# Kernel optimization log

Hardware: AMD Instinct MI355X
Metric: run time of the kernel (lower is better)

The kernel has to match this reference:

```python
import jax, jax.numpy as jnp
import numpy as np

D = 768          # 16*16*3
N = 196
H = 8
HD = D // H      # 96
SCALE = HD ** -0.5
EPS = 1e-5


def _ln(x, s, b):
    m = jnp.mean(x, axis=-1, keepdims=True)
    v = jnp.mean((x - m) ** 2, axis=-1, keepdims=True)
    return (x - m) * jax.lax.rsqrt(v + EPS) * s + b


def setup_inputs() -> dict:
    key = jax.random.key(0)
    ks = jax.random.split(key, 16)
    B = 64
    w = lambda k, shp: (jax.random.normal(k, shp, jnp.float32) * 0.02)
    return {
        "x": jax.random.normal(ks[0], (B, N, D), jnp.float32),
        "x_Eem": jax.random.normal(ks[1], (B, 3, 222, 222), jnp.float32),
        "pos_emb": jax.random.normal(ks[2], (1, N, D), jnp.float32),
        "dw_w": w(ks[3], (3, 1, 16, 16)),     # depthwise conv, groups=3 (OIHW, I=1)
        "dw_b": jnp.zeros((3,), jnp.float32),
        "pw_w": w(ks[4], (D, 3)),             # pointwise 1x1 conv as matrix
        "pw_b": jnp.zeros((D,), jnp.float32),
        "qkv_w": w(ks[5], (3 * D, D)),        # no bias (qkv_bias=False)
        "proj_w": w(ks[6], (D, D)),
        "proj_b": jnp.zeros((D,), jnp.float32),
        "ln1_s": jnp.ones((D,), jnp.float32),
        "ln1_b": jnp.zeros((D,), jnp.float32),
        "ln2_s": jnp.ones((D,), jnp.float32),
        "ln2_b": jnp.zeros((D,), jnp.float32),
        "fc1_w": w(ks[7], (4 * D, D)),
        "fc1_b": jnp.zeros((4 * D,), jnp.float32),
        "fc2_w": w(ks[8], (D, 4 * D)),
        "fc2_b": jnp.zeros((D,), jnp.float32),
    }


def _patch_embed(img, dw_w, dw_b, pw_w, pw_b):
    # depthwise conv: kernel 16, stride 16, padding 1, groups=3
    h = jax.lax.conv_general_dilated(
        img, dw_w, window_strides=(16, 16), padding=[(1, 1), (1, 1)],
        dimension_numbers=("NCHW", "OIHW", "NCHW"), feature_group_count=3)
    h = h + dw_b[None, :, None, None]           # [B,3,14,14]
    h = jnp.einsum("bchw,oc->bohw", h, pw_w) + pw_b[None, :, None, None]
    B = h.shape[0]
    return h.reshape(B, D, N).transpose(0, 2, 1)  # [B,N,D]


def _ve_attention(x, x_emb, qkv_w, proj_w, proj_b):
    B = x.shape[0]
    # pooling gates (AdaptiveMax/AvgPool2d on 3D input pools last two dims)
    maxg = jnp.max(x, axis=(1, 2), keepdims=True)       # [B,1,1]
    maxn = jnp.max(x, axis=2, keepdims=True)            # [B,N,1]
    aveg = jnp.mean(x, axis=(1, 2), keepdims=True)      # [B,1,1]
    aven = jnp.mean(x, axis=2, keepdims=True)           # [B,N,1]
    # F.softmax(maxg*maxn, dim=1); F.softmax(aveg*aven) -> default dim=0 for 3D input
    gate = jax.nn.softmax(maxg * maxn, axis=1) * jax.nn.softmax(aveg * aven, axis=0)
    qkv = jnp.einsum("bnd,ed->bne", x, qkv_w)            # [B,N,3D]
    q = qkv[:, :, :D]
    k = qkv[:, :, D:2 * D]
    v = qkv[:, :, 2 * D:] * gate + x_emb
    to_h = lambda t: t.reshape(B, N, H, HD).transpose(0, 2, 1, 3)  # [B,H,N,hd]
    q, k, v = to_h(q), to_h(k), to_h(v)
    # scores = (q@k^T + v@k^T) * scale == ((q+v)@k^T) * scale
    attn = jax.nn.softmax(jnp.einsum("bhnd,bhmd->bhnm", q + v, k) * SCALE, axis=-1)
    out = jnp.einsum("bhnm,bhmd->bhnd", attn, v)
    out = out.transpose(0, 2, 1, 3).reshape(B, N, D)
    return jnp.einsum("bnd,ed->bne", out, proj_w) + proj_b


def reference(x, x_Eem, pos_emb, dw_w, dw_b, pw_w, pw_b, qkv_w, proj_w, proj_b,
              ln1_s, ln1_b, ln2_s, ln2_b, fc1_w, fc1_b, fc2_w, fc2_b):
    x_emb = _patch_embed(x_Eem, dw_w, dw_b, pw_w, pw_b)
    x = x + pos_emb
    x = x + _ve_attention(_ln(x, ln1_s, ln1_b), x_emb, qkv_w, proj_w, proj_b)
    h = _ln(x, ln2_s, ln2_b)
    h = jax.nn.gelu(jnp.einsum("bnd,fd->bnf", h, fc1_w) + fc1_b, approximate=False)
    h = jnp.einsum("bnf,df->bnd", h, fc2_w) + fc2_b
    return x + h
```

## Files before the change

### kernel.cpp

```cpp
#include <hip/hip_runtime.h>

#define DEV __device__ __forceinline__

typedef __attribute__((ext_vector_type(8))) short short8_t;
typedef __attribute__((ext_vector_type(4))) float float4_t;
typedef __attribute__((ext_vector_type(4))) unsigned short ushort4_t;
typedef __attribute__((ext_vector_type(8))) unsigned short ushort8_t;

#define ATT_SCALE 0.10206207261596577f

DEV unsigned short f2bf(float f) {
  unsigned u = __float_as_uint(f);
  u += 0x7fffu + ((u >> 16) & 1u);
  return (unsigned short)(u >> 16);
}
DEV float bf2f(unsigned short h) { return __uint_as_float(((unsigned)h) << 16); }

DEV float4_t mfma16(short8_t a, short8_t b, float4_t c) {
  return __builtin_amdgcn_mfma_f32_16x16x32_bf16(a, b, c, 0, 0, 0);
}

DEV void gl_lds16(const void* g, void* l) {
  __builtin_amdgcn_global_load_lds((__attribute__((address_space(1))) void*)g,
                                   (__attribute__((address_space(3))) void*)l, 16, 0, 0);
}

__global__ __launch_bounds__(256) void cvt_kernel(const float* __restrict__ w0,
    const float* __restrict__ w1, const float* __restrict__ w2, const float* __restrict__ w3,
    unsigned short* __restrict__ d0, unsigned short* __restrict__ d1,
    unsigned short* __restrict__ d2, unsigned short* __restrict__ d3) {
  const int i = blockIdx.x * 256 + threadIdx.x;
  const float* s;
  unsigned short* d;
  int j;
  if (i < 442368) { s = w0; d = d0; j = i; }
  else if (i < 589824) { s = w1; d = d1; j = i - 442368; }
  else if (i < 1179648) { s = w2; d = d2; j = i - 589824; }
  else { s = w3; d = d3; j = i - 1179648; }
  float4_t v = ((const float4_t*)s)[j];
  ushort4_t o = {f2bf(v[0]), f2bf(v[1]), f2bf(v[2]), f2bf(v[3])};
  ((ushort4_t*)d)[j] = o;
}

__global__ __launch_bounds__(256) void dwconv_kernel(const float* __restrict__ img,
    const float* __restrict__ wgt, const float* __restrict__ wb, float* __restrict__ h3) {
  __shared__ float wsm[256];
  const int bc = blockIdx.x;
  const int c = bc % 3;
  const int tid = threadIdx.x;
  wsm[tid] = wgt[c * 256 + tid];
  __syncthreads();
  if (tid < 196) {
    const int ph = tid / 14, pwv = tid % 14;
    const float* ip = img + (size_t)bc * (222 * 222);
    float acc = 0.f;
#pragma unroll
    for (int i = 0; i < 16; ++i) {
      const int r = ph * 16 - 1 + i;
      if ((unsigned)r < 222u) {
        const float* rp = ip + r * 222;
#pragma unroll
        for (int j = 0; j < 16; ++j) {
          const int cc = pwv * 16 - 1 + j;
          if ((unsigned)cc < 222u) acc += rp[cc] * wsm[i * 16 + j];
        }
      }
    }
    h3[(size_t)bc * 196 + tid] = acc + wb[c];
  }
}

__global__ __launch_bounds__(256) void ln1_kernel(const float* __restrict__ x,
    const float* __restrict__ pos, const float* __restrict__ sG, const float* __restrict__ bG,
    unsigned short* __restrict__ xln, float* __restrict__ maxn, float* __restrict__ aven) {
  __shared__ float rA[4], rB[4], rC[4], rD[4];
  const int row = blockIdx.x, tid = threadIdx.x;
  const int n = row % 196;
  const float* xr = x + (size_t)row * 768;
  const float* pr = pos + (size_t)n * 768;
  float v0 = xr[tid] + pr[tid];
  float v1 = xr[tid + 256] + pr[tid + 256];
  float v2 = xr[tid + 512] + pr[tid + 512];
  float sm = v0 + v1 + v2;
  float sq = v0 * v0 + v1 * v1 + v2 * v2;
  for (int o = 32; o; o >>= 1) { sm += __shfl_xor(sm, o); sq += __shfl_xor(sq, o); }
  if ((tid & 63) == 0) { rA[tid >> 6] = sm; rB[tid >> 6] = sq; }
  __syncthreads();
  const float mean = (rA[0] + rA[1] + rA[2] + rA[3]) * (1.f / 768.f);
  const float var = (rB[0] + rB[1] + rB[2] + rB[3]) * (1.f / 768.f) - mean * mean;
  const float rstd = rsqrtf(var + 1e-5f);
  float y0 = (v0 - mean) * rstd * sG[tid] + bG[tid];
  float y1 = (v1 - mean) * rstd * sG[tid + 256] + bG[tid + 256];
  float y2 = (v2 - mean) * rstd * sG[tid + 512] + bG[tid + 512];
  unsigned short* xo = xln + (size_t)row * 768;
  xo[tid] = f2bf(y0); xo[tid + 256] = f2bf(y1); xo[tid + 512] = f2bf(y2);
  float mx = fmaxf(y0, fmaxf(y1, y2));
  float sy = y0 + y1 + y2;
  for (int o = 32; o; o >>= 1) { mx = fmaxf(mx, __shfl_xor(mx, o)); sy += __shfl_xor(sy, o); }
  if ((tid & 63) == 0) { rC[tid >> 6] = mx; rD[tid >> 6] = sy; }
  __syncthreads();
  if (tid == 0) {
    maxn[row] = fmaxf(fmaxf(rC[0], rC[1]), fmaxf(rC[2], rC[3]));
    aven[row] = (rD[0] + rD[1] + rD[2] + rD[3]) * (1.f / 768.f);
  }
}

__global__ __launch_bounds__(256) void ln2_kernel(const float* __restrict__ x2,
    const float* __restrict__ sG, const float* __restrict__ bG, unsigned short* __restrict__ h2) {
  __shared__ float rA[4], rB[4];
  const int row = blockIdx.x, tid = threadIdx.x;
  const float* xr = x2 + (size_t)row * 768;
  float v0 = xr[tid], v1 = xr[tid + 256], v2 = xr[tid + 512];
  float sm = v0 + v1 + v2;
  float sq = v0 * v0 + v1 * v1 + v2 * v2;
  for (int o = 32; o; o >>= 1) { sm += __shfl_xor(sm, o); sq += __shfl_xor(sq, o); }
  if ((tid & 63) == 0) { rA[tid >> 6] = sm; rB[tid >> 6] = sq; }
  __syncthreads();
  const float mean = (rA[0] + rA[1] + rA[2] + rA[3]) * (1.f / 768.f);
  const float var = (rB[0] + rB[1] + rB[2] + rB[3]) * (1.f / 768.f) - mean * mean;
  const float rstd = rsqrtf(var + 1e-5f);
  unsigned short* xo = h2 + (size_t)row * 768;
  xo[tid]       = f2bf((v0 - mean) * rstd * sG[tid] + bG[tid]);
  xo[tid + 256] = f2bf((v1 - mean) * rstd * sG[tid + 256] + bG[tid + 256]);
  xo[tid + 512] = f2bf((v2 - mean) * rstd * sG[tid + 512] + bG[tid + 512]);
}

__global__ __launch_bounds__(256) void gate1_kernel(const float* __restrict__ maxn,
    const float* __restrict__ aven, float* __restrict__ aveg, float* __restrict__ s1) {
  __shared__ float rA[4], rB[4], rC[4], rD[4];
  const int b = blockIdx.x, tid = threadIdx.x;
  const bool ok = tid < 196;
  const float mv = ok ? maxn[b * 196 + tid] : -1e30f;
  const float av = ok ? aven[b * 196 + tid] : 0.f;
  float m = mv, sa = av;
  for (int o = 32; o; o >>= 1) { m = fmaxf(m, __shfl_xor(m, o)); sa += __shfl_xor(sa, o); }
  if ((tid & 63) == 0) { rA[tid >> 6] = m; rB[tid >> 6] = sa; }
  __syncthreads();
  const float maxg = fmaxf(fmaxf(rA[0], rA[1]), fmaxf(rA[2], rA[3]));
  const float avg = (rB[0] + rB[1] + rB[2] + rB[3]) * (1.f / 196.f);
  if (tid == 0) aveg[b] = avg;
  const float t1 = ok ? maxg * mv : -1e30f;
  float m2 = t1;
  for (int o = 32; o; o >>= 1) m2 = fmaxf(m2, __shfl_xor(m2, o));
  if ((tid & 63) == 0) rC[tid >> 6] = m2;
  __syncthreads();
  const float m2g = fmaxf(fmaxf(rC[0], rC[1]), fmaxf(rC[2], rC[3]));
  const float e = ok ? __expf(t1 - m2g) : 0.f;
  float se = e;
  for (int o = 32; o; o >>= 1) se += __shfl_xor(se, o);
  if ((tid & 63) == 0) rD[tid >> 6] = se;
  __syncthreads();
  const float seg = rD[0] + rD[1] + rD[2] + rD[3];
  if (ok) s1[b * 196 + tid] = e / seg;
}

__global__ __launch_bounds__(64) void gate2_kernel(const float* __restrict__ aveg,
    const float* __restrict__ aven, const float* __restrict__ s1, float* __restrict__ gate) {
  const int n = blockIdx.x, bb = threadIdx.x;
  const float t2 = aveg[bb] * aven[bb * 196 + n];
  float m = t2;
  for (int o = 32; o; o >>= 1) m = fmaxf(m, __shfl_xor(m, o));
  const float e = __expf(t2 - m);
  float ssum = e;
  for (int o = 32; o; o >>= 1) ssum += __shfl_xor(ssum, o);
  gate[bb * 196 + n] = s1[bb * 196 + n] * e / ssum;
}

enum { M_QKV = 0, M_PROJ = 1, M_GELU = 2, M_FC2 = 3 };

template <int MODE>
__global__ __launch_bounds__(256, 2) void gemm_bt(
    const unsigned short* __restrict__ A, const unsigned short* __restrict__ W,
    int K, int Nd,
    const float* __restrict__ bias,
    const float* __restrict__ res0, const float* __restrict__ res1,
    const float* __restrict__ gate, const float* __restrict__ h3,
    const float* __restrict__ pw, const float* __restrict__ pwb,
    unsigned short* __restrict__ oQ, unsigned short* __restrict__ oK,
    unsigned short* __restrict__ oV,
    float* __restrict__ oF, unsigned short* __restrict__ oB) {
  __shared__ __align__(16) unsigned short smem[8192];
  const int tid = threadIdx.x;
  const int w = tid >> 6, lane = tid & 63;
  const int l15 = lane & 15, quad = lane >> 4;
  const int n0 = blockIdx.x * 128, m0 = blockIdx.y * 128;

  const int row0 = tid >> 2;
  const int kc = (((tid & 3) ^ ((tid >> 3) & 3)) << 3);
  const size_t arow0 = (size_t)(m0 + row0) * K + kc;
  const size_t arow1 = (size_t)(m0 + 64 + row0) * K + kc;
  const size_t brow0 = (size_t)(n0 + row0) * K + kc;
  const size_t brow1 = (size_t)(n0 + 64 + row0) * K + kc;
  char* sb = (char*)smem;
  const int ldsA0 = w * 1024, ldsA1 = 4096 + w * 1024;
  const int ldsB0 = 8192 + w * 1024, ldsB1 = 12288 + w * 1024;

  float4_t acc[4][4];
#pragma unroll
  for (int i = 0; i < 4; ++i)
#pragma unroll
    for (int j = 0; j < 4; ++j) acc[i][j] = (float4_t){0.f, 0.f, 0.f, 0.f};

  const int wm = (w >> 1) << 6, wn = (w & 1) << 6;
  const unsigned short* as_ = smem;
  const unsigned short* bs_ = smem + 4096;
  const int squad = quad ^ ((l15 >> 1) & 3);

  for (int kt = 0; kt < K; kt += 32) {
    gl_lds16(A + arow0 + kt, sb + ldsA0);
    gl_lds16(A + arow1 + kt, sb + ldsA1);
    gl_lds16(W + brow0 + kt, sb + ldsB0);
    gl_lds16(W + brow1 + kt, sb + ldsB1);
    __syncthreads();
    short8_t af[4], bfr[4];
#pragma unroll
    for (int mi = 0; mi < 4; ++mi)
      af[mi] = *(const short8_t*)(as_ + (wm + mi * 16 + l15) * 32 + squad * 8);
#pragma unroll
    for (int ni = 0; ni < 4; ++ni)
      bfr[ni] = *(const short8_t*)(bs_ + (wn + ni * 16 + l15) * 32 + squad * 8);
#pragma unroll
    for (int mi = 0; mi < 4; ++mi)
#pragma unroll
      for (int ni = 0; ni < 4; ++ni)
        acc[mi][ni] = mfma16(bfr[ni], af[mi], acc[mi][ni]);
    __syncthreads();
  }

  if (MODE == M_QKV) {
    const int sel = n0 / 768;
    unsigned short* dst = (sel == 0) ? oQ : (sel == 1) ? oK : oV;
    const int nb = n0 - sel * 768 + wn;
#pragma unroll
    for (int mi = 0; mi < 4; ++mi) {
      const int m = m0 + wm + mi * 16 + l15;
      float gv = 0.f, h30 = 0.f, h31 = 0.f, h32 = 0.f;
      if (sel == 2) {
        const int b = m / 196, n = m - b * 196;
        gv = gate[m];
        h30 = h3[(b * 3 + 0) * 196 + n];
        h31 = h3[(b * 3 + 1) * 196 + n];
        h32 = h3[(b * 3 + 2) * 196 + n];
      }
      unsigned short* orow = dst + (size_t)m * 768;
#pragma unroll
      for (int ni = 0; ni < 4; ++ni) {
        const int dcol = nb + ni * 16 + quad * 4;
        ushort4_t st;
        if (sel == 2) {
          const float4_t pwf0 = *(const float4_t*)(pw + dcol * 3);
          const float4_t pwf1 = *(const float4_t*)(pw + dcol * 3 + 4);
          const float4_t pwf2 = *(const float4_t*)(pw + dcol * 3 + 8);
          const float4_t pbf = *(const float4_t*)(pwb + dcol);
          float pwflat[12] = {pwf0[0], pwf0[1], pwf0[2], pwf0[3], pwf1[0], pwf1[1],
                              pwf1[2], pwf1[3], pwf2[0], pwf2[1], pwf2[2], pwf2[3]};
#pragma unroll
          for (int r = 0; r < 4; ++r) {
            const float v = acc[mi][ni][r] * gv + h30 * pwflat[3 * r] +
                            h31 * pwflat[3 * r + 1] + h32 * pwflat[3 * r + 2] + pbf[r];
            st[r] = f2bf(v);
          }
        } else {
#pragma unroll
          for (int r = 0; r < 4; ++r) st[r] = f2bf(acc[mi][ni][r]);
        }
        *(ushort4_t*)(orow + dcol) = st;
      }
    }
  } else if (MODE == M_PROJ || MODE == M_FC2) {
#pragma unroll
    for (int mi = 0; mi < 4; ++mi) {
      const int m = m0 + wm + mi * 16 + l15;
      const int nseq = m % 196;
      const float* rr0 = res0 + (size_t)m * 768;
      const float* rr1 = (MODE == M_PROJ) ? res1 + (size_t)nseq * 768 : nullptr;
      float* oo = oF + (size_t)m * 768;
#pragma unroll
      for (int ni = 0; ni < 4; ++ni) {
        const int col = n0 + wn + ni * 16 + quad * 4;
        const float4_t bb = *(const float4_t*)(bias + col);
        const float4_t r0v = *(const float4_t*)(rr0 + col);
        float4_t v;
#pragma unroll
        for (int r = 0; r < 4; ++r) v[r] = acc[mi][ni][r] + bb[r] + r0v[r];
        if (MODE == M_PROJ) {
          const float4_t r1v = *(const float4_t*)(rr1 + col);
#pragma unroll
          for (int r = 0; r < 4; ++r) v[r] += r1v[r];
        }
        *(float4_t*)(oo + col) = v;
      }
    }
  } else {
#pragma unroll
    for (int mi = 0; mi < 4; ++mi) {
      const int m = m0 + wm + mi * 16 + l15;
      unsigned short* oo = oB + (size_t)m * Nd;
#pragma unroll
      for (int ni = 0; ni < 4; ++ni) {
        const int col = n0 + wn + ni * 16 + quad * 4;
        const float4_t bb = *(const float4_t*)(bias + col);
        ushort4_t st;
#pragma unroll
        for (int r = 0; r < 4; ++r) {
          const float t = acc[mi][ni][r] + bb[r];
          st[r] = f2bf(0.5f * t * (1.f + erff(t * 0.70710678118654752f)));
        }
        *(ushort4_t*)(oo + col) = st;
      }
    }
  }
}

__global__ __launch_bounds__(256) void vtrans_kernel(const unsigned short* __restrict__ vg,
                                                     unsigned short* __restrict__ vt) {
  __shared__ unsigned short lds[96 * 226];
  const int bh = blockIdx.x, b = bh >> 3, h = bh & 7;
  const int tid = threadIdx.x;
  const unsigned short* base = vg + (size_t)(b * 196) * 768 + h * 96;
  for (int idx = tid; idx < 196 * 12; idx += 256) {
    const int n = idx / 12, c = idx % 12;
    const ushort8_t rv = *(const ushort8_t*)(base + (size_t)n * 768 + c * 8);
#pragma unroll
    for (int j = 0; j < 8; ++j) lds[(c * 8 + j) * 226 + n] = rv[j];
  }
  __syncthreads();
  unsigned short* ob = vt + (size_t)bh * (96 * 224);
  for (int idx = tid; idx < 96 * 28; idx += 256) {
    const int d = idx / 28, c = idx % 28;
    const int nn = c * 8;
    ushort8_t o;
#pragma unroll
    for (int j = 0; j < 8; ++j) o[j] = (nn + j < 196) ? lds[d * 226 + nn + j] : (unsigned short)0;
    *(ushort8_t*)(ob + (size_t)d * 224 + nn) = o;
  }
}

__global__ __launch_bounds__(256, 2) void attn_kernel(
    const unsigned short* __restrict__ qg, const unsigned short* __restrict__ vg,
    const unsigned short* __restrict__ kg, const unsigned short* __restrict__ vt,
    unsigned short* __restrict__ att) {
  __shared__ __align__(16) unsigned short p_s[4][16][232];
  const int bh = blockIdx.x, b = bh >> 3, h = bh & 7;
  const int tid = threadIdx.x, w = tid >> 6, lane = tid & 63;
  const int l15 = lane & 15, quad = lane >> 4;
  const unsigned short* qb = qg + (size_t)(b * 196) * 768 + h * 96;
  const unsigned short* vb = vg + (size_t)(b * 196) * 768 + h * 96;
  const unsigned short* kb = kg + (size_t)(b * 196) * 768 + h * 96;
  const unsigned short* vtb = vt + (size_t)bh * (96 * 224);
  for (int i = lane; i < 256; i += 64) p_s[w][i >> 4][208 + (i & 15)] = 0;

  for (int qt = w; qt < 13; qt += 4) {
    const size_t qoff = (size_t)(qt * 16 + l15) * 768 + quad * 8;
    short8_t a0, a1, a2;
    {
      const ushort8_t q0 = *(const ushort8_t*)(qb + qoff);
      const ushort8_t q1 = *(const ushort8_t*)(qb + qoff + 32);
      const ushort8_t q2 = *(const ushort8_t*)(qb + qoff + 64);
      const ushort8_t v0 = *(const ushort8_t*)(vb + qoff);
      const ushort8_t v1 = *(const ushort8_t*)(vb + qoff + 32);
      const ushort8_t v2 = *(const ushort8_t*)(vb + qoff + 64);
#pragma unroll
      for (int j = 0; j < 8; ++j) {
        a0[j] = (short)f2bf(bf2f(q0[j]) + bf2f(v0[j]));
        a1[j] = (short)f2bf(bf2f(q1[j]) + bf2f(v1[j]));
        a2[j] = (short)f2bf(bf2f(q2[j]) + bf2f(v2[j]));
      }
    }
    float4_t S[13];
#pragma unroll
    for (int c = 0; c < 13; ++c) S[c] = (float4_t){0.f, 0.f, 0.f, 0.f};
#pragma unroll
    for (int c = 0; c < 13; ++c) {
      const unsigned short* kr = kb + (size_t)(c * 16 + l15) * 768 + quad * 8;
      S[c] = mfma16(a0, *(const short8_t*)(kr), S[c]);
      S[c] = mfma16(a1, *(const short8_t*)(kr + 32), S[c]);
      S[c] = mfma16(a2, *(const short8_t*)(kr + 64), S[c]);
    }
    float mx[4] = {-1e30f, -1e30f, -1e30f, -1e30f};
#pragma unroll
    for (int c = 0; c < 13; ++c) {
      const bool okc = (c * 16 + l15) < 196;
#pragma unroll
      for (int r = 0; r < 4; ++r) {
        const float v = S[c][r] * ATT_SCALE;
        S[c][r] = okc ? v : -1e30f;
        mx[r] = fmaxf(mx[r], S[c][r]);
      }
    }
#pragma unroll
    for (int o = 1; o <= 8; o <<= 1)
#pragma unroll
      for (int r = 0; r < 4; ++r) mx[r] = fmaxf(mx[r], __shfl_xor(mx[r], o));
    float sum[4] = {0.f, 0.f, 0.f, 0.f};
#pragma unroll
    for (int c = 0; c < 13; ++c)
#pragma unroll
      for (int r = 0; r < 4; ++r) {
        const float e = __expf(S[c][r] - mx[r]);
        S[c][r] = e;
        sum[r] += e;
      }
#pragma unroll
    for (int o = 1; o <= 8; o <<= 1)
#pragma unroll
      for (int r = 0; r < 4; ++r) sum[r] += __shfl_xor(sum[r], o);
    float inv[4];
#pragma unroll
    for (int r = 0; r < 4; ++r) inv[r] = 1.f / sum[r];
#pragma unroll
    for (int c = 0; c < 13; ++c)
#pragma unroll
      for (int r = 0; r < 4; ++r)
        p_s[w][quad * 4 + r][c * 16 + l15] = f2bf(S[c][r] * inv[r]);

    float4_t O[6];
#pragma unroll
    for (int ni = 0; ni < 6; ++ni) O[ni] = (float4_t){0.f, 0.f, 0.f, 0.f};
#pragma unroll
    for (int s = 0; s < 7; ++s) {
      short8_t pa = *(const short8_t*)(&p_s[w][l15][s * 32 + quad * 8]);
#pragma unroll
      for (int ni = 0; ni < 6; ++ni) {
        short8_t vf = *(const short8_t*)(vtb + (size_t)(ni * 16 + l15) * 224 + s * 32 + quad * 8);
        O[ni] = mfma16(vf, pa, O[ni]);
      }
    }
    const int m = qt * 16 + l15;
    if (m < 196) {
      unsigned short* ar = att + (size_t)(b * 196 + m) * 768 + h * 96 + quad * 4;
#pragma unroll
      for (int ni = 0; ni < 6; ++ni) {
        ushort4_t st = {f2bf(O[ni][0]), f2bf(O[ni][1]), f2bf(O[ni][2]), f2bf(O[ni][3])};
        *(ushort4_t*)(ar + ni * 16) = st;
      }
    }
  }
}

extern "C" void kernel_launch(void* const* d_in, const int* in_sizes, int n_in,
                              void* d_out, int out_size, void* d_ws, size_t ws_size,
                              hipStream_t stream) {
  (void)in_sizes; (void)n_in; (void)out_size; (void)ws_size;
  const float* x      = (const float*)d_in[0];
  const float* xE     = (const float*)d_in[1];
  const float* pos    = (const float*)d_in[2];
  const float* dw_w   = (const float*)d_in[3];
  const float* dw_b   = (const float*)d_in[4];
  const float* pw_w   = (const float*)d_in[5];
  const float* pw_b   = (const float*)d_in[6];
  const float* qkv_w  = (const float*)d_in[7];
  const float* proj_w = (const float*)d_in[8];
  const float* proj_b = (const float*)d_in[9];
  const float* ln1_s  = (const float*)d_in[10];
  const float* ln1_b  = (const float*)d_in[11];
  const float* ln2_s  = (const float*)d_in[12];
  const float* ln2_b  = (const float*)d_in[13];
  const float* fc1_w  = (const float*)d_in[14];
  const float* fc1_b  = (const float*)d_in[15];
  const float* fc2_w  = (const float*)d_in[16];
  const float* fc2_b  = (const float*)d_in[17];
  float* out = (float*)d_out;

  char* ws = (char*)d_ws;
  size_t off = 0;
  auto alloc = [&](size_t bytes) -> void* {
    void* p = ws + off;
    off += (bytes + 255) & ~(size_t)255;
    return p;
  };
  unsigned short* wqkv  = (unsigned short*)alloc(1769472ull * 2);
  unsigned short* wproj = (unsigned short*)alloc(589824ull * 2);
  unsigned short* wfc1  = (unsigned short*)alloc(2359296ull * 2);
  unsigned short* wfc2  = (unsigned short*)alloc(2359296ull * 2);
  float* h3   = (float*)alloc(37632ull * 4);
  unsigned short* xln = (unsigned short*)alloc(9633792ull * 2);
  float* maxn = (float*)alloc(12544ull * 4);
  float* aven = (float*)alloc(12544ull * 4);
  float* aveg = (float*)alloc(64ull * 4);
  float* s1   = (float*)alloc(12544ull * 4);
  float* gate = (float*)alloc(12544ull * 4);
  const size_t ROWP = 9646080ull;
  unsigned short* big = (unsigned short*)alloc((3ull * ROWP + 11010048ull) * 2);
  unsigned short* qg = big;
  unsigned short* kg = big + ROWP;
  unsigned short* vg = big + 2ull * ROWP;
  unsigned short* vt = big + 3ull * ROWP;
  unsigned short* att  = xln;
  unsigned short* h2   = xln;
  unsigned short* gbuf = big;
  float* x2 = out;

  cvt_kernel<<<dim3(6912), 256, 0, stream>>>(qkv_w, proj_w, fc1_w, fc2_w, wqkv, wproj, wfc1, wfc2);
  dwconv_kernel<<<dim3(192), 256, 0, stream>>>(xE, dw_w, dw_b, h3);
  ln1_kernel<<<dim3(12544), 256, 0, stream>>>(x, pos, ln1_s, ln1_b, xln, maxn, aven);
  gate1_kernel<<<dim3(64), 256, 0, stream>>>(maxn, aven, aveg, s1);
  gate2_kernel<<<dim3(196), 64, 0, stream>>>(aveg, aven, s1, gate);
  gemm_bt<M_QKV><<<dim3(18, 98), 256, 0, stream>>>(xln, wqkv, 768, 2304, nullptr, nullptr, nullptr,
      gate, h3, pw_w, pw_b, qg, kg, vg, nullptr, nullptr);
  vtrans_kernel<<<dim3(512), 256, 0, stream>>>(vg, vt);
  attn_kernel<<<dim3(512), 256, 0, stream>>>(qg, vg, kg, vt, att);
  gemm_bt<M_PROJ><<<dim3(6, 98), 256, 0, stream>>>(att, wproj, 768, 768, proj_b, x, pos,
      nullptr, nullptr, nullptr, nullptr, nullptr, nullptr, nullptr, x2, nullptr);
  ln2_kernel<<<dim3(12544), 256, 0, stream>>>(x2, ln2_s, ln2_b, h2);
  gemm_bt<M_GELU><<<dim3(24, 98), 256, 0, stream>>>(h2, wfc1, 768, 3072, fc1_b, nullptr, nullptr,
      nullptr, nullptr, nullptr, nullptr, nullptr, nullptr, nullptr, nullptr, gbuf);
  gemm_bt<M_FC2><<<dim3(6, 98), 256, 0, stream>>>(gbuf, wfc2, 3072, 768, fc2_b, x2, nullptr,
      nullptr, nullptr, nullptr, nullptr, nullptr, nullptr, nullptr, out, nullptr);
}
```

Before: 626.9 us.

## Use K=64 GEMM tiles with XCD-aware tile remap and per-wave attention blocks

```diff
diff --git a/kernel.cpp b/kernel.cpp
--- a/kernel.cpp
+++ b/kernel.cpp
@@ -171,7 +171,7 @@
 template <int MODE>
 __global__ __launch_bounds__(256, 2) void gemm_bt(
     const unsigned short* __restrict__ A, const unsigned short* __restrict__ W,
-    int K, int Nd,
+    int K, int Nd, int NT, int T,
     const float* __restrict__ bias,
     const float* __restrict__ res0, const float* __restrict__ res1,
     const float* __restrict__ gate, const float* __restrict__ h3,
@@ -179,21 +179,28 @@
     unsigned short* __restrict__ oQ, unsigned short* __restrict__ oK,
     unsigned short* __restrict__ oV,
     float* __restrict__ oF, unsigned short* __restrict__ oB) {
-  __shared__ __align__(16) unsigned short smem[8192];
+  __shared__ __align__(16) unsigned short smem[16384];
+  const int l = blockIdx.x;
+  const int xc = l & 7, kb = l >> 3;
+  const int tbase = (xc * T) >> 3;
+  if (kb >= (((xc + 1) * T) >> 3) - tbase) return;
+  const int t = tbase + kb;
+  const int mt = t / NT, nt = t - mt * NT;
+  const int m0 = mt * 128, n0 = nt * 128;
+
   const int tid = threadIdx.x;
   const int w = tid >> 6, lane = tid & 63;
   const int l15 = lane & 15, quad = lane >> 4;
-  const int n0 = blockIdx.x * 128, m0 = blockIdx.y * 128;
-
-  const int row0 = tid >> 2;
-  const int kc = (((tid & 3) ^ ((tid >> 3) & 3)) << 3);
-  const size_t arow0 = (size_t)(m0 + row0) * K + kc;
-  const size_t arow1 = (size_t)(m0 + 64 + row0) * K + kc;
-  const size_t brow0 = (size_t)(n0 + row0) * K + kc;
-  const size_t brow1 = (size_t)(n0 + 64 + row0) * K + kc;
+
+  const int srow = w * 8 + (lane >> 3);
+  const int cs = (lane & 7) ^ (lane >> 3);
+  size_t aoff[4], boff[4];
+#pragma unroll
+  for (int j = 0; j < 4; ++j) {
+    aoff[j] = (size_t)(m0 + j * 32 + srow) * K + cs * 8;
+    boff[j] = (size_t)(n0 + j * 32 + srow) * K + cs * 8;
+  }
   char* sb = (char*)smem;
-  const int ldsA0 = w * 1024, ldsA1 = 4096 + w * 1024;
-  const int ldsB0 = 8192 + w * 1024, ldsB1 = 12288 + w * 1024;
 
   float4_t acc[4][4];
 #pragma unroll
@@ -203,27 +210,31 @@
 
   const int wm = (w >> 1) << 6, wn = (w & 1) << 6;
   const unsigned short* as_ = smem;
-  const unsigned short* bs_ = smem + 4096;
-  const int squad = quad ^ ((l15 >> 1) & 3);
-
-  for (int kt = 0; kt < K; kt += 32) {
-    gl_lds16(A + arow0 + kt, sb + ldsA0);
-    gl_lds16(A + arow1 + kt, sb + ldsA1);
-    gl_lds16(W + brow0 + kt, sb + ldsB0);
-    gl_lds16(W + brow1 + kt, sb + ldsB1);
+  const unsigned short* bs_ = smem + 8192;
+  const int rx = l15 & 7;
+
+  for (int kt = 0; kt < K; kt += 64) {
+#pragma unroll
+    for (int j = 0; j < 4; ++j) gl_lds16(A + aoff[j] + kt, sb + j * 4096 + w * 1024);
+#pragma unroll
+    for (int j = 0; j < 4; ++j) gl_lds16(W + boff[j] + kt, sb + 16384 + j * 4096 + w * 1024);
     __syncthreads();
-    short8_t af[4], bfr[4];
-#pragma unroll
-    for (int mi = 0; mi < 4; ++mi)
-      af[mi] = *(const short8_t*)(as_ + (wm + mi * 16 + l15) * 32 + squad * 8);
-#pragma unroll
-    for (int ni = 0; ni < 4; ++ni)
-      bfr[ni] = *(const short8_t*)(bs_ + (wn + ni * 16 + l15) * 32 + squad * 8);
-#pragma unroll
-    for (int mi = 0; mi < 4; ++mi)
+#pragma unroll
+    for (int h = 0; h < 2; ++h) {
+      const int ch = (quad + 4 * h) ^ rx;
+      short8_t af[4], bfr[4];
+#pragma unroll
+      for (int mi = 0; mi < 4; ++mi)
+        af[mi] = *(const short8_t*)(as_ + (wm + mi * 16 + l15) * 64 + ch * 8);
 #pragma unroll
       for (int ni = 0; ni < 4; ++ni)
-        acc[mi][ni] = mfma16(bfr[ni], af[mi], acc[mi][ni]);
+        bfr[ni] = *(const short8_t*)(bs_ + (wn + ni * 16 + l15) * 64 + ch * 8);
+#pragma unroll
+      for (int mi = 0; mi < 4; ++mi)
+#pragma unroll
+        for (int ni = 0; ni < 4; ++ni)
+          acc[mi][ni] = mfma16(bfr[ni], af[mi], acc[mi][ni]);
+    }
     __syncthreads();
   }
 
@@ -303,8 +314,8 @@
         ushort4_t st;
 #pragma unroll
         for (int r = 0; r < 4; ++r) {
-          const float t = acc[mi][ni][r] + bb[r];
-          st[r] = f2bf(0.5f * t * (1.f + erff(t * 0.70710678118654752f)));
+          const float t2 = acc[mi][ni][r] + bb[r];
+          st[r] = f2bf(0.5f * t2 * (1.f + erff(t2 * 0.70710678118654752f)));
         }
         *(ushort4_t*)(oo + col) = st;
       }
@@ -341,99 +352,109 @@
     const unsigned short* __restrict__ kg, const unsigned short* __restrict__ vt,
     unsigned short* __restrict__ att) {
   __shared__ __align__(16) unsigned short p_s[4][16][232];
-  const int bh = blockIdx.x, b = bh >> 3, h = bh & 7;
   const int tid = threadIdx.x, w = tid >> 6, lane = tid & 63;
   const int l15 = lane & 15, quad = lane >> 4;
+  const int l = blockIdx.x;
+  const int bt = (l & 7) * 208 + (l >> 3);
+  const int t = bt * 4 + w;
+  const int bh = t / 13, qt = t - bh * 13;
+  const int b = bh >> 3, h = bh & 7;
   const unsigned short* qb = qg + (size_t)(b * 196) * 768 + h * 96;
   const unsigned short* vb = vg + (size_t)(b * 196) * 768 + h * 96;
   const unsigned short* kb = kg + (size_t)(b * 196) * 768 + h * 96;
   const unsigned short* vtb = vt + (size_t)bh * (96 * 224);
   for (int i = lane; i < 256; i += 64) p_s[w][i >> 4][208 + (i & 15)] = 0;
 
-  for (int qt = w; qt < 13; qt += 4) {
-    const size_t qoff = (size_t)(qt * 16 + l15) * 768 + quad * 8;
-    short8_t a0, a1, a2;
-    {
-      const ushort8_t q0 = *(const ushort8_t*)(qb + qoff);
-      const ushort8_t q1 = *(const ushort8_t*)(qb + qoff + 32);
-      const ushort8_t q2 = *(const ushort8_t*)(qb + qoff + 64);
-      const ushort8_t v0 = *(const ushort8_t*)(vb + qoff);
-      const ushort8_t v1 = *(const ushort8_t*)(vb + qoff + 32);
-      const ushort8_t v2 = *(const ushort8_t*)(vb + qoff + 64);
-#pragma unroll
-      for (int j = 0; j < 8; ++j) {
-        a0[j] = (short)f2bf(bf2f(q0[j]) + bf2f(v0[j]));
-        a1[j] = (short)f2bf(bf2f(q1[j]) + bf2f(v1[j]));
-        a2[j] = (short)f2bf(bf2f(q2[j]) + bf2f(v2[j]));
-      }
-    }
-    float4_t S[13];
-#pragma unroll
-    for (int c = 0; c < 13; ++c) S[c] = (float4_t){0.f, 0.f, 0.f, 0.f};
-#pragma unroll
-    for (int c = 0; c < 13; ++c) {
-      const unsigned short* kr = kb + (size_t)(c * 16 + l15) * 768 + quad * 8;
-      S[c] = mfma16(a0, *(const short8_t*)(kr), S[c]);
-      S[c] = mfma16(a1, *(const short8_t*)(kr + 32), S[c]);
-      S[c] = mfma16(a2, *(const short8_t*)(kr + 64), S[c]);
-    }
-    float mx[4] = {-1e30f, -1e30f, -1e30f, -1e30f};
-#pragma unroll
-    for (int c = 0; c < 13; ++c) {
-      const bool okc = (c * 16 + l15) < 196;
-#pragma unroll
-      for (int r = 0; r < 4; ++r) {
-        const float v = S[c][r] * ATT_SCALE;
-        S[c][r] = okc ? v : -1e30f;
-        mx[r] = fmaxf(mx[r], S[c][r]);
-      }
-    }
-#pragma unroll
-    for (int o = 1; o <= 8; o <<= 1)
-#pragma unroll
-      for (int r = 0; r < 4; ++r) mx[r] = fmaxf(mx[r], __shfl_xor(mx[r], o));
-    float sum[4] = {0.f, 0.f, 0.f, 0.f};
-#pragma unroll
-    for (int c = 0; c < 13; ++c)
-#pragma unroll
-      for (int r = 0; r < 4; ++r) {
-        const float e = __expf(S[c][r] - mx[r]);
-        S[c][r] = e;
-        sum[r] += e;
-      }
-#pragma unroll
-    for (int o = 1; o <= 8; o <<= 1)
-#pragma unroll
-      for (int r = 0; r < 4; ++r) sum[r] += __shfl_xor(sum[r], o);
-    float inv[4];
-#pragma unroll
-    for (int r = 0; r < 4; ++r) inv[r] = 1.f / sum[r];
-#pragma unroll
-    for (int c = 0; c < 13; ++c)
-#pragma unroll
-      for (int r = 0; r < 4; ++r)
-        p_s[w][quad * 4 + r][c * 16 + l15] = f2bf(S[c][r] * inv[r]);
-
-    float4_t O[6];
-#pragma unroll
-    for (int ni = 0; ni < 6; ++ni) O[ni] = (float4_t){0.f, 0.f, 0.f, 0.f};
-#pragma unroll
-    for (int s = 0; s < 7; ++s) {
-      short8_t pa = *(const short8_t*)(&p_s[w][l15][s * 32 + quad * 8]);
-#pragma unroll
-      for (int ni = 0; ni < 6; ++ni) {
-        short8_t vf = *(const short8_t*)(vtb + (size_t)(ni * 16 + l15) * 224 + s * 32 + quad * 8);
-        O[ni] = mfma16(vf, pa, O[ni]);
-      }
-    }
-    const int m = qt * 16 + l15;
+  const size_t qoff = (size_t)(qt * 16 + l15) * 768 + quad * 8;
+  short8_t a0, a1, a2;
+  {
+    const ushort8_t q0 = *(const ushort8_t*)(qb + qoff);
+    const ushort8_t q1 = *(const ushort8_t*)(qb + qoff + 32);
+    const ushort8_t q2 = *(const ushort8_t*)(qb + qoff + 64);
+    const ushort8_t v0 = *(const ushort8_t*)(vb + qoff);
+    const ushort8_t v1 = *(const ushort8_t*)(vb + qoff + 32);
+    const ushort8_t v2 = *(const ushort8_t*)(vb + qoff + 64);
+#pragma unroll
+    for (int j = 0; j < 8; ++j) {
+      a0[j] = (short)f2bf(bf2f(q0[j]) + bf2f(v0[j]));
+      a1[j] = (short)f2bf(bf2f(q1[j]) + bf2f(v1[j]));
+      a2[j] = (short)f2bf(bf2f(q2[j]) + bf2f(v2[j]));
+    }
+  }
+  float4_t S[13];
+#pragma unroll
+  for (int c = 0; c < 13; ++c) S[c] = (float4_t){0.f, 0.f, 0.f, 0.f};
+#pragma unroll
+  for (int c = 0; c < 13; ++c) {
+    const unsigned short* kr = kb + (size_t)(c * 16 + l15) * 768 + quad * 8;
+    S[c] = mfma16(a0, *(const short8_t*)(kr), S[c]);
+    S[c] = mfma16(a1, *(const short8_t*)(kr + 32), S[c]);
+    S[c] = mfma16(a2, *(const short8_t*)(kr + 64), S[c]);
+  }
+  float mx[4] = {-1e30f, -1e30f, -1e30f, -1e30f};
+#pragma unroll
+  for (int c = 0; c < 13; ++c) {
+    const bool okc = (c * 16 + l15) < 196;
+#pragma unroll
+    for (int r = 0; r < 4; ++r) {
+      const float v = S[c][r] * ATT_SCALE;
+      S[c][r] = okc ? v : -1e30f;
+      mx[r] = fmaxf(mx[r], S[c][r]);
+    }
+  }
+#pragma unroll
+  for (int o = 1; o <= 8; o <<= 1)
+#pragma unroll
+    for (int r = 0; r < 4; ++r) mx[r] = fmaxf(mx[r], __shfl_xor(mx[r], o));
+  float sum[4] = {0.f, 0.f, 0.f, 0.f};
+#pragma unroll
+  for (int c = 0; c < 13; ++c)
+#pragma unroll
+    for (int r = 0; r < 4; ++r) {
+      const float e = __expf(S[c][r] - mx[r]);
+      S[c][r] = e;
+      sum[r] += e;
+    }
+#pragma unroll
+  for (int o = 1; o <= 8; o <<= 1)
+#pragma unroll
+    for (int r = 0; r < 4; ++r) sum[r] += __shfl_xor(sum[r], o);
+  float inv[4];
+#pragma unroll
+  for (int r = 0; r < 4; ++r) inv[r] = 1.f / sum[r];
+#pragma unroll
+  for (int c = 0; c < 13; ++c)
+#pragma unroll
+    for (int r = 0; r < 4; ++r)
+      p_s[w][quad * 4 + r][c * 16 + l15] = f2bf(S[c][r] * inv[r]);
+
+  float4_t O[6];
+#pragma unroll
+  for (int ni = 0; ni < 6; ++ni) O[ni] = (float4_t){0.f, 0.f, 0.f, 0.f};
+#pragma unroll
+  for (int s = 0; s < 7; ++s) {
+    short8_t pa = *(const short8_t*)(&p_s[w][l15][s * 32 + quad * 8]);
+#pragma unroll
+    for (int ni = 0; ni < 6; ++ni) {
+      short8_t vf = *(const short8_t*)(vtb + (size_t)(ni * 16 + l15) * 224 + s * 32 + quad * 8);
+      O[ni] = mfma16(vf, pa, O[ni]);
+    }
+  }
+#pragma unroll
+  for (int ni = 0; ni < 6; ++ni) {
+    ushort4_t st = {f2bf(O[ni][0]), f2bf(O[ni][1]), f2bf(O[ni][2]), f2bf(O[ni][3])};
+    *(ushort4_t*)(&p_s[w][l15][ni * 16 + quad * 4]) = st;
+  }
+  __asm__ volatile("s_waitcnt lgkmcnt(0)");
+  unsigned short* ab = att + (size_t)(b * 196) * 768 + h * 96;
+#pragma unroll
+  for (int p = 0; p < 3; ++p) {
+    const int idx = p * 64 + lane;
+    const int row = idx / 12, c16 = idx - row * 12;
+    const int m = qt * 16 + row;
     if (m < 196) {
-      unsigned short* ar = att + (size_t)(b * 196 + m) * 768 + h * 96 + quad * 4;
-#pragma unroll
-      for (int ni = 0; ni < 6; ++ni) {
-        ushort4_t st = {f2bf(O[ni][0]), f2bf(O[ni][1]), f2bf(O[ni][2]), f2bf(O[ni][3])};
-        *(ushort4_t*)(ar + ni * 16) = st;
-      }
+      const ushort8_t o = *(const ushort8_t*)(&p_s[w][row][c16 * 8]);
+      *(ushort8_t*)(ab + (size_t)m * 768 + c16 * 8) = o;
     }
   }
 }
@@ -496,15 +517,17 @@
   ln1_kernel<<<dim3(12544), 256, 0, stream>>>(x, pos, ln1_s, ln1_b, xln, maxn, aven);
   gate1_kernel<<<dim3(64), 256, 0, stream>>>(maxn, aven, aveg, s1);
   gate2_kernel<<<dim3(196), 64, 0, stream>>>(aveg, aven, s1, gate);
-  gemm_bt<M_QKV><<<dim3(18, 98), 256, 0, stream>>>(xln, wqkv, 768, 2304, nullptr, nullptr, nullptr,
-      gate, h3, pw_w, pw_b, qg, kg, vg, nullptr, nullptr);
+  gemm_bt<M_QKV><<<dim3(1768), 256, 0, stream>>>(xln, wqkv, 768, 2304, 18, 1764,
+      nullptr, nullptr, nullptr, gate, h3, pw_w, pw_b, qg, kg, vg, nullptr, nullptr);
   vtrans_kernel<<<dim3(512), 256, 0, stream>>>(vg, vt);
-  attn_kernel<<<dim3(512), 256, 0, stream>>>(qg, vg, kg, vt, att);
-  gemm_bt<M_PROJ><<<dim3(6, 98), 256, 0, stream>>>(att, wproj, 768, 768, proj_b, x, pos,
-      nullptr, nullptr, nullptr, nullptr, nullptr, nullptr, nullptr, x2, nullptr);
+  attn_kernel<<<dim3(1664), 256, 0, stream>>>(qg, vg, kg, vt, att);
+  gemm_bt<M_PROJ><<<dim3(592), 256, 0, stream>>>(att, wproj, 768, 768, 6, 588,
+      proj_b, x, pos, nullptr, nullptr, nullptr, nullptr, nullptr, nullptr, nullptr, x2, nullptr);
   ln2_kernel<<<dim3(12544), 256, 0, stream>>>(x2, ln2_s, ln2_b, h2);
-  gemm_bt<M_GELU><<<dim3(24, 98), 256, 0, stream>>>(h2, wfc1, 768, 3072, fc1_b, nullptr, nullptr,
-      nullptr, nullptr, nullptr, nullptr, nullptr, nullptr, nullptr, nullptr, gbuf);
-  gemm_bt<M_FC2><<<dim3(6, 98), 256, 0, stream>>>(gbuf, wfc2, 3072, 768, fc2_b, x2, nullptr,
-      nullptr, nullptr, nullptr, nullptr, nullptr, nullptr, nullptr, out, nullptr);
-}
+  gemm_bt<M_GELU><<<dim3(2352), 256, 0, stream>>>(h2, wfc1, 768, 3072, 24, 2352,
+      fc1_b, nullptr, nullptr, nullptr, nullptr, nullptr, nullptr, nullptr, nullptr, nullptr,
+      nullptr, gbuf);
+  gemm_bt<M_FC2><<<dim3(592), 256, 0, stream>>>(gbuf, wfc2, 3072, 768, 6, 588,
+      fc2_b, x2, nullptr, nullptr, nullptr, nullptr, nullptr, nullptr, nullptr, nullptr, out,
+      nullptr);
+}
```

Measured after the change: 520.3 us. -17.0%, faster.
